# Kernel optimization log

Measured on AMD Instinct MI355X. Metric: run time of the kernel, lower is better.

Reference implementation:

```python
import jax, jax.numpy as jnp
import numpy as np

B, T, C, H = 16, 512, 256, 8
HS_T = C // H   # temporal head size = 32
HS_S = T // H   # spatial head size = 64
EPS = 1e-6


def _ln(x, w, b):
    m = x.mean(-1, keepdims=True)
    v = ((x - m) ** 2).mean(-1, keepdims=True)
    return (x - m) / jnp.sqrt(v + EPS) * w + b


def setup_inputs() -> dict:
    key = jax.random.key(0)
    ks = jax.random.split(key, 16)
    rn = lambda k, s, scale: jax.random.normal(k, s, dtype=jnp.float32) * scale
    inp = {
        "x_T": rn(ks[0], (B, T, C), 1.0),
        "x_S": rn(ks[1], (B, C, T), 1.0),
        # temporal attention: per-head q/k/v projections, stacked [H, hs, C]
        "Wq_t": rn(ks[2], (H, HS_T, C), C ** -0.5),
        "Wk_t": rn(ks[3], (H, HS_T, C), C ** -0.5),
        "Wv_t": rn(ks[4], (H, HS_T, C), C ** -0.5),
        "Wo": rn(ks[5], (C, C), C ** -0.5),
        # spatial attention: per-head q/k over the time axis, stacked [H, hs_s, T]
        "Wq_s": rn(ks[6], (H, HS_S, T), T ** -0.5),
        "Wk_s": rn(ks[7], (H, HS_S, T), T ** -0.5),
        # feed-forward blocks (expansion_factor=4)
        "ff1_w1": rn(ks[8], (4 * C, C), C ** -0.5),
        "ff1_b1": jnp.zeros((4 * C,), jnp.float32),
        "ff1_w2": rn(ks[9], (C, 4 * C), (4 * C) ** -0.5),
        "ff1_b2": jnp.zeros((C,), jnp.float32),
        "ff2_w1": rn(ks[10], (4 * C, C), C ** -0.5),
        "ff2_b1": jnp.zeros((4 * C,), jnp.float32),
        "ff2_w2": rn(ks[11], (C, 4 * C), (4 * C) ** -0.5),
        "ff2_b2": jnp.zeros((C,), jnp.float32),
        # layernorm affine params
        "t_ln1_w": jnp.ones((C,), jnp.float32), "t_ln1_b": jnp.zeros((C,), jnp.float32),
        "t_ln2_w": jnp.ones((C,), jnp.float32), "t_ln2_b": jnp.zeros((C,), jnp.float32),
        "s_ln1_w": jnp.ones((T,), jnp.float32), "s_ln1_b": jnp.zeros((T,), jnp.float32),
        "fus_ln_w": jnp.ones((C,), jnp.float32), "fus_ln_b": jnp.zeros((C,), jnp.float32),
    }
    return inp


def reference(x_T, x_S, Wq_t, Wk_t, Wv_t, Wo, Wq_s, Wk_s,
              ff1_w1, ff1_b1, ff1_w2, ff1_b2, ff2_w1, ff2_b1, ff2_w2, ff2_b2,
              t_ln1_w, t_ln1_b, t_ln2_w, t_ln2_b, s_ln1_w, s_ln1_b,
              fus_ln_w, fus_ln_b):
    # ---- temporal (causal) multi-head attention ----
    h = _ln(x_T, t_ln1_w, t_ln1_b)                         # [B,T,C]
    q = jnp.einsum('btc,hdc->bhtd', h, Wq_t)
    k = jnp.einsum('btc,hdc->bhtd', h, Wk_t)
    v = jnp.einsum('btc,hdc->bhtd', h, Wv_t)
    scores = jnp.einsum('bhtd,bhsd->bhts', q, k) / jnp.sqrt(jnp.float32(HS_T))
    causal = jnp.tril(jnp.ones((T, T), dtype=bool))
    scores = jnp.where(causal, scores, -jnp.inf)
    att = jax.nn.softmax(scores, axis=-1)
    o = jnp.einsum('bhts,bhsd->bhtd', att, v)              # [B,H,T,hs]
    o = o.transpose(0, 2, 1, 3).reshape(B, T, C)           # concat heads
    attn_out = o @ Wo.T
    x = x_T + attn_out
    # FFN 1
    h2 = _ln(x, t_ln2_w, t_ln2_b)
    f = jax.nn.relu(h2 @ ff1_w1.T + ff1_b1) @ ff1_w2.T + ff1_b2
    temporal_out = x + f                                   # [B,T,C]
    # ---- spatial (non-causal) attention over neurons ----
    hs = _ln(x_S, s_ln1_w, s_ln1_b)                        # [B,C,T]
    qs = jnp.einsum('bct,hdt->bhcd', hs, Wq_s)
    ks = jnp.einsum('bct,hdt->bhcd', hs, Wk_s)
    sc = jnp.einsum('bhcd,bhed->bhce', qs, ks) / jnp.sqrt(jnp.float32(HS_S))
    spatial_weights = jax.nn.softmax(sc, axis=-1).mean(axis=1)   # [B,C,C], mean over heads
    # ---- fusion ----
    fused = jnp.einsum('bce,bte->btc', spatial_weights, temporal_out)
    x2 = temporal_out + fused
    h3 = _ln(x2, fus_ln_w, fus_ln_b)
    f2 = jax.nn.relu(h3 @ ff2_w1.T + ff2_b1) @ ff2_w2.T + ff2_b2
    out = x2 + f2
    return out, spatial_weights
```

## Files before the change

### kernel.cpp

```cpp
#include <hip/hip_runtime.h>
#include <hip/hip_bf16.h>

typedef __hip_bfloat16 bf16;
typedef __attribute__((ext_vector_type(8))) short short8;
typedef __attribute__((ext_vector_type(4))) float f32x4;

#define F_BIAS 1
#define F_RELU 2
#define F_RES  4

__device__ __forceinline__ void st_out(float* p, float v){ *p = v; }
__device__ __forceinline__ void st_out(bf16* p, float v){ *p = __float2bfloat16(v); }
__device__ __forceinline__ short f2bs(float f){
  bf16 h = __float2bfloat16(f);
  return *reinterpret_cast<short*>(&h);
}

__device__ __forceinline__ void gl_lds16(const void* g, void* l){
  __builtin_amdgcn_global_load_lds(
      (const __attribute__((address_space(1))) void*)g,
      (__attribute__((address_space(3))) void*)l, 16, 0, 0);
}

struct ProArgs {
  const float* wsrc[10];
  bf16* wdst[10];
  const float *xT, *xS, *tl1w, *tl1b, *sl1w, *sl1b;
  bf16 *hT, *hS;
};

__device__ void ln_body(bf16* __restrict__ dst, const float* __restrict__ src,
                        const float* __restrict__ w, const float* __restrict__ bvec,
                        int row, int rowLen){
  int tid = threadIdx.x;
  const float* s = src + (size_t)row*rowLen;
  float x0 = s[tid];
  float x1 = (rowLen > 256) ? s[tid+256] : 0.0f;
  float sum = x0 + x1, sq = x0*x0 + x1*x1;
  #pragma unroll
  for (int off=32; off; off>>=1){
    sum += __shfl_down(sum, off, 64);
    sq  += __shfl_down(sq , off, 64);
  }
  __shared__ float sbs[4], sbq[4];
  int wid = tid>>6, lane = tid&63;
  if (lane==0){ sbs[wid]=sum; sbq[wid]=sq; }
  __syncthreads();
  if (tid==0){
    float a=0, b2=0;
    for (int i=0;i<4;i++){ a+=sbs[i]; b2+=sbq[i]; }
    sbs[0]=a; sbq[0]=b2;
  }
  __syncthreads();
  float inv  = 1.0f/(float)rowLen;
  float mean = sbs[0]*inv;
  float var  = sbq[0]*inv - mean*mean;
  float rstd = rsqrtf(var + 1e-6f);
  bf16* d = dst + (size_t)row*rowLen;
  d[tid] = __float2bfloat16((x0-mean)*rstd*w[tid] + bvec[tid]);
  if (rowLen > 256)
    d[tid+256] = __float2bfloat16((x1-mean)*rstd*w[tid+256] + bvec[tid+256]);
}

__global__ __launch_bounds__(256) void prologue(ProArgs a){
  int blk = blockIdx.x;
  if (blk < 1792){
    int v = blk*256 + threadIdx.x;
    int e = v*4;
    int seg = (e>=65536)+(e>=131072)+(e>=196608)+(e>=262144)+(e>=524288)
            + (e>=786432)+(e>=1048576)+(e>=1310720)+(e>=1572864);
    const int starts[10] = {0,65536,131072,196608,262144,524288,786432,
                            1048576,1310720,1572864};
    int off = e - starts[seg];
    float4 f = *(const float4*)(a.wsrc[seg] + off);
    short4 o;
    o.x = f2bs(f.x); o.y = f2bs(f.y); o.z = f2bs(f.z); o.w = f2bs(f.w);
    *(short4*)((short*)a.wdst[seg] + off) = o;
  } else if (blk < 1792 + 8192){
    ln_body(a.hT, a.xT, a.tl1w, a.tl1b, blk-1792, 256);
  } else {
    ln_body(a.hS, a.xS, a.sl1w, a.sl1b, blk-9984, 512);
  }
}

template<int BM, int BK>
__device__ __forceinline__ void gemm_body(
    const bf16* __restrict__ A, const bf16* __restrict__ B,
    float* __restrict__ outF, bf16* __restrict__ outB,
    const float* __restrict__ bias, const float* __restrict__ resid,
    int K, int lda, int ldb, int ldc, int flags, int m0, int n0){
  __shared__ short As[BM*BK];
  __shared__ short Bs[128*BK];
  int tid = threadIdx.x;
  int w = tid>>6, lane = tid&63, quad = lane>>4, l16 = lane&15;
  constexpr int WM = BM/2;
  constexpr int MF = WM/16;
  constexpr int CPR = BK/8;
  constexpr int CA = BM*CPR/256;
  constexpr int CB = 128*CPR/256;
  int wm = (w>>1)*WM, wn = (w&1)*64;
  f32x4 acc[MF][4];
  #pragma unroll
  for (int r=0;r<MF;r++)
    #pragma unroll
    for (int j=0;j<4;j++)
      acc[r][j] = (f32x4){0.f,0.f,0.f,0.f};

  for (int k0 = 0; k0 < K; k0 += BK){
    #pragma unroll
    for (int c=0;c<CA;c++){
      int ch = tid + c*256;
      int row = ch / CPR, p = ch % CPR;
      gl_lds16(A + (size_t)(m0+row)*lda + k0 + ((p ^ (row&(CPR-1)))*8),
               &As[row*BK + p*8]);
    }
    #pragma unroll
    for (int c=0;c<CB;c++){
      int ch = tid + c*256;
      int row = ch / CPR, p = ch % CPR;
      gl_lds16(B + (size_t)(n0+row)*ldb + k0 + ((p ^ (row&(CPR-1)))*8),
               &Bs[row*BK + p*8]);
    }
    __syncthreads();
    #pragma unroll
    for (int ks=0; ks<BK/32; ++ks){
      short8 af[MF], bfr[4];
      #pragma unroll
      for (int r=0;r<MF;r++){
        int rr = wm + r*16 + l16;
        af[r] = *(short8*)&As[rr*BK + (((ks*4+quad) ^ (rr&(CPR-1)))*8)];
      }
      #pragma unroll
      for (int j=0;j<4;j++){
        int rr = wn + j*16 + l16;
        bfr[j] = *(short8*)&Bs[rr*BK + (((ks*4+quad) ^ (rr&(CPR-1)))*8)];
      }
      #pragma unroll
      for (int r=0;r<MF;r++)
        #pragma unroll
        for (int j=0;j<4;j++)
          acc[r][j] = __builtin_amdgcn_mfma_f32_16x16x32_bf16(af[r], bfr[j], acc[r][j], 0,0,0);
    }
    __syncthreads();
  }
  #pragma unroll
  for (int r=0;r<MF;r++){
    int mb = m0 + wm + r*16 + quad*4;
    #pragma unroll
    for (int j=0;j<4;j++){
      int n = n0 + wn + j*16 + l16;
      float bv = (flags & F_BIAS) ? bias[n] : 0.0f;
      #pragma unroll
      for (int e=0;e<4;e++){
        float v = acc[r][j][e] + bv;
        if (flags & F_RELU) v = fmaxf(v, 0.0f);
        long long idx = (long long)(mb+e)*ldc + n;
        if (flags & F_RES) v += resid[idx];
        if (outF) outF[idx] = v;
        if (outB) st_out(outB + idx, v);
      }
    }
  }
}

template<int BM, int BK>
__global__ __launch_bounds__(256) void gemm_mfma(
    const bf16* __restrict__ A, const bf16* __restrict__ B,
    float* __restrict__ outF, bf16* __restrict__ outB,
    const float* __restrict__ bias, const float* __restrict__ resid,
    int K, int lda, int ldb, int ldc, int flags){
  gemm_body<BM,BK>(A,B,outF,outB,bias,resid,K,lda,ldb,ldc,flags,
                   blockIdx.x*BM, blockIdx.y*128);
}

struct GArgs {
  const bf16 *A, *B;
  float* outF; bf16* outB;
  const float *bias, *resid;
  int K, lda, ldb, ldc, flags, ty;
};
__global__ __launch_bounds__(256) void gemm_dual(GArgs g0, GArgs g1, int n0){
  int id = blockIdx.x;
  bool first = id < n0;
  const GArgs& g = first ? g0 : g1;
  int t = first ? id : id - n0;
  int bx = t / g.ty, by = t - bx*g.ty;
  gemm_body<128,64>(g.A, g.B, g.outF, g.outB, g.bias, g.resid,
                    g.K, g.lda, g.ldb, g.ldc, g.flags, bx*128, by*128);
}

__global__ __launch_bounds__(256) void gemm_ln(
    const bf16* __restrict__ A, const bf16* __restrict__ B,
    float* __restrict__ outF, bf16* __restrict__ outLN,
    const float* __restrict__ resid,
    const float* __restrict__ lnw, const float* __restrict__ lnb,
    int K, int lda, int ldb, int flags,
    long long sA, long long sB, long long sO, long long sR){
  int bz = blockIdx.z;
  A += (size_t)bz*sA;
  B += (size_t)bz*sB;
  long long obase = (long long)bz*sO;
  __shared__ short As[32*64];
  __shared__ short Bs[256*64];
  __shared__ float redS[2][32], redQ[2][32];
  int tid = threadIdx.x;
  int m0 = blockIdx.x*32;
  int w = tid>>6, lane = tid&63, quad = lane>>4, l16 = lane&15;
  int wm = (w>>1)*16, wn = (w&1)*128;
  f32x4 acc[8];
  #pragma unroll
  for (int j=0;j<8;j++) acc[j] = (f32x4){0.f,0.f,0.f,0.f};

  for (int k0 = 0; k0 < K; k0 += 64){
    {
      int row = tid >> 3, p = tid & 7;
      gl_lds16(A + (size_t)(m0+row)*lda + k0 + ((p ^ (row&7))*8),
               &As[row*64 + p*8]);
    }
    #pragma unroll
    for (int c=0;c<8;c++){
      int ch = tid + c*256;
      int row = ch >> 3, p = ch & 7;
      gl_lds16(B + (size_t)row*ldb + k0 + ((p ^ (row&7))*8),
               &Bs[row*64 + p*8]);
    }
    __syncthreads();
    #pragma unroll
    for (int ks=0; ks<2; ++ks){
      int rr = wm + l16;
      short8 af = *(short8*)&As[rr*64 + (((ks*4+quad) ^ (rr&7))*8)];
      #pragma unroll
      for (int j=0;j<8;j++){
        int rb = wn + j*16 + l16;
        short8 bfr = *(short8*)&Bs[rb*64 + (((ks*4+quad) ^ (rb&7))*8)];
        acc[j] = __builtin_amdgcn_mfma_f32_16x16x32_bf16(af, bfr, acc[j], 0,0,0);
      }
    }
    __syncthreads();
  }
  #pragma unroll
  for (int e=0;e<4;e++){
    int row = wm + quad*4 + e;
    float s = 0.f, q2 = 0.f;
    #pragma unroll
    for (int j=0;j<8;j++){
      float v = acc[j][e];
      if (flags & F_RES)
        v += resid[(long long)bz*sR + (long long)(m0+row)*256 + wn + j*16 + l16];
      acc[j][e] = v;
      s += v; q2 += v*v;
    }
    #pragma unroll
    for (int off=1; off<16; off<<=1){
      s  += __shfl_xor(s , off, 16);
      q2 += __shfl_xor(q2, off, 16);
    }
    if (l16==0){ redS[w&1][row] = s; redQ[w&1][row] = q2; }
  }
  __syncthreads();
  #pragma unroll
  for (int e=0;e<4;e++){
    int row = wm + quad*4 + e;
    float tot = redS[0][row] + redS[1][row];
    float tq  = redQ[0][row] + redQ[1][row];
    float mean = tot * (1.0f/256.0f);
    float var  = tq * (1.0f/256.0f) - mean*mean;
    float rstd = rsqrtf(var + 1e-6f);
    #pragma unroll
    for (int j=0;j<8;j++){
      int col = wn + j*16 + l16;
      float v = acc[j][e];
      long long idx = obase + (long long)(m0+row)*256 + col;
      if (outF) outF[idx] = v;
      outLN[idx] = __float2bfloat16((v-mean)*rstd*lnw[col] + lnb[col]);
    }
  }
}

__device__ __forceinline__ int fsw(int row){ return (row>>1)&3; }
__global__ __launch_bounds__(256) void flash_mfma(
    const bf16* __restrict__ qkv, bf16* __restrict__ o){
  int qt = (int)gridDim.x - 1 - (int)blockIdx.x;
  int h = blockIdx.y, b = blockIdx.z;
  int tid = threadIdx.x;
  int w = tid>>6, lane = tid&63, quad = lane>>4, l16 = lane&15;
  __shared__ bf16 Qs[64*32];
  __shared__ bf16 Ks[64*32];
  __shared__ bf16 Vt[32*72];
  __shared__ bf16 Ps[64*72];
  const bf16* base = qkv + (size_t)b*512*768;
  int t0 = qt*64;
  int srow = tid>>2, spos = tid&3;
  gl_lds16(base + (size_t)(t0+srow)*768 + h*32 + ((spos ^ fsw(srow))*8),
           &Qs[srow*32 + spos*8]);
  f32x4 accO[2];
  accO[0] = (f32x4){0.f,0.f,0.f,0.f};
  accO[1] = (f32x4){0.f,0.f,0.f,0.f};
  float m_i[4], l_i[4];
  #pragma unroll
  for (int e=0;e<4;e++){ m_i[e] = -3.0e38f; l_i[e] = 0.0f; }
  const float scale = 0.17677669529663687f;

  for (int kt = 0; kt <= qt; ++kt){
    int s0 = kt*64;
    __syncthreads();
    {
      const bf16* rp = base + (size_t)(s0+srow)*768 + h*32;
      gl_lds16(rp + 256 + ((spos ^ fsw(srow))*8), &Ks[srow*32 + spos*8]);
      short8 v = *(const short8*)(rp + 512 + spos*8);
      #pragma unroll
      for (int q=0;q<8;q++){
        short tmp = v[q];
        Vt[(spos*8+q)*72 + srow] = *(bf16*)&tmp;
      }
    }
    __syncthreads();
    int rq = w*16 + l16;
    short8 aq = *(short8*)&Qs[rq*32 + ((quad ^ fsw(rq))*8)];
    f32x4 S[4];
    #pragma unroll
    for (int j2=0;j2<4;j2++){
      int rk = j2*16 + l16;
      short8 bk = *(short8*)&Ks[rk*32 + ((quad ^ fsw(rk))*8)];
      S[j2] = __builtin_amdgcn_mfma_f32_16x16x32_bf16(aq, bk,
                (f32x4){0.f,0.f,0.f,0.f}, 0,0,0);
    }
    bool diag = (kt == qt);
    int qrow_base = t0 + w*16 + quad*4;
    #pragma unroll
    for (int e=0;e<4;e++){
      float sv[4];
      #pragma unroll
      for (int j2=0;j2<4;j2++){
        float x = S[j2][e]*scale;
        if (diag && (s0 + j2*16 + l16 > qrow_base + e)) x = -3.0e38f;
        sv[j2] = x;
      }
      float mx = fmaxf(fmaxf(sv[0],sv[1]), fmaxf(sv[2],sv[3]));
      #pragma unroll
      for (int off=1; off<16; off<<=1) mx = fmaxf(mx, __shfl_xor(mx, off, 64));
      float m_new = fmaxf(m_i[e], mx);
      float alpha = __expf(m_i[e]-m_new);
      float rs = 0.0f;
      #pragma unroll
      for (int j2=0;j2<4;j2++){
        float p = __expf(sv[j2]-m_new);
        rs += p;
        Ps[(w*16+quad*4+e)*72 + j2*16 + l16] = __float2bfloat16(p);
      }
      #pragma unroll
      for (int off=1; off<16; off<<=1) rs += __shfl_xor(rs, off, 64);
      l_i[e] = l_i[e]*alpha + rs;
      m_i[e] = m_new;
      accO[0][e] *= alpha;
      accO[1][e] *= alpha;
    }
    __syncthreads();
    #pragma unroll
    for (int sh=0; sh<2; ++sh){
      short8 ap = *(short8*)&Ps[(w*16+l16)*72 + sh*32 + quad*8];
      #pragma unroll
      for (int dh=0; dh<2; ++dh){
        short8 bv = *(short8*)&Vt[(dh*16+l16)*72 + sh*32 + quad*8];
        accO[dh] = __builtin_amdgcn_mfma_f32_16x16x32_bf16(ap, bv, accO[dh], 0,0,0);
      }
    }
  }
  #pragma unroll
  for (int e=0;e<4;e++){
    float inv = 1.0f/l_i[e];
    int t = t0 + w*16 + quad*4 + e;
    bf16* op = o + ((size_t)(b*512+t))*256 + h*32 + l16;
    op[0]  = __float2bfloat16(accO[0][e]*inv);
    op[16] = __float2bfloat16(accO[1][e]*inv);
  }
}

__device__ void spatial_body(const bf16* __restrict__ qk,
                             float* __restrict__ out1, bf16* __restrict__ swB,
                             int ct, int b){
  int tid = threadIdx.x;
  int w = tid>>6, lane = tid&63, quad = lane>>4, l16 = lane&15;
  __shared__ bf16 Qall[16*512];
  __shared__ bf16 Ks[256*64];
  __shared__ float redM[4][16], redS2[4][16];
  const bf16* qbase = qk + ((size_t)(b*256 + ct*16))*1024;
  #pragma unroll
  for (int c=0;c<4;c++){
    int ch = tid + c*256;
    int row = ch>>6, p = ch&63;
    gl_lds16(qbase + (size_t)row*1024 + ((p ^ (row&7))*8), &Qall[row*512 + p*8]);
  }
  float fRes[4][4];
  #pragma unroll
  for (int j=0;j<4;j++)
    #pragma unroll
    for (int e=0;e<4;e++) fRes[j][e] = 0.0f;

  for (int h=0; h<8; ++h){
    __syncthreads();
    #pragma unroll
    for (int c=0;c<8;c++){
      int ch = tid + c*256;
      int e = ch>>3, p = ch&7;
      gl_lds16(qk + ((size_t)(b*256 + e))*1024 + 512 + h*64 + ((p ^ (e&7))*8),
               &Ks[e*64 + p*8]);
    }
    __syncthreads();
    f32x4 acc[4];
    #pragma unroll
    for (int j=0;j<4;j++) acc[j] = (f32x4){0.f,0.f,0.f,0.f};
    #pragma unroll
    for (int ks=0; ks<2; ++ks){
      int g = h*8 + ks*4 + quad;
      short8 aq = *(short8*)&Qall[l16*512 + ((g ^ (l16&7))*8)];
      #pragma unroll
      for (int j=0;j<4;j++){
        int e = w*64 + j*16 + l16;
        short8 bk = *(short8*)&Ks[e*64 + (((ks*4+quad) ^ (e&7))*8)];
        acc[j] = __builtin_amdgcn_mfma_f32_16x16x32_bf16(aq, bk, acc[j], 0,0,0);
      }
    }
    #pragma unroll
    for (int e=0;e<4;e++){
      float m = -3.0e38f;
      #pragma unroll
      for (int j=0;j<4;j++){
        float s = acc[j][e]*0.125f;
        acc[j][e] = s;
        m = fmaxf(m, s);
      }
      #pragma unroll
      for (int off=1; off<16; off<<=1) m = fmaxf(m, __shfl_xor(m, off, 16));
      if (l16==0) redM[w][quad*4+e] = m;
    }
    __syncthreads();
    #pragma unroll
    for (int e=0;e<4;e++){
      int r = quad*4+e;
      float m = fmaxf(fmaxf(redM[0][r],redM[1][r]), fmaxf(redM[2][r],redM[3][r]));
      float s = 0.0f;
      #pragma unroll
      for (int j=0;j<4;j++){
        float p = __expf(acc[j][e]-m);
        acc[j][e] = p; s += p;
      }
      #pragma unroll
      for (int off=1; off<16; off<<=1) s += __shfl_xor(s, off, 16);
      if (l16==0) redS2[w][r] = s;
    }
    __syncthreads();
    #pragma unroll
    for (int e=0;e<4;e++){
      int r = quad*4+e;
      float tot = redS2[0][r]+redS2[1][r]+redS2[2][r]+redS2[3][r];
      float inv = 0.125f/tot;
      #pragma unroll
      for (int j=0;j<4;j++) fRes[j][e] += acc[j][e]*inv;
    }
  }
  #pragma unroll
  for (int e=0;e<4;e++){
    int c = ct*16 + quad*4 + e;
    size_t rb = ((size_t)b*256 + c)*256;
    #pragma unroll
    for (int j=0;j<4;j++){
      int col = w*64 + j*16 + l16;
      out1[rb+col] = fRes[j][e];
      swB[rb+col]  = __float2bfloat16(fRes[j][e]);
    }
  }
}

__global__ __launch_bounds__(256) void mixed_l2(
    const bf16* __restrict__ gA, const bf16* __restrict__ gB,
    float* __restrict__ gOutF, bf16* __restrict__ gOutB,
    const float* __restrict__ gBias, const float* __restrict__ gResid,
    const bf16* __restrict__ qk, float* __restrict__ out1,
    bf16* __restrict__ swB){
  int id = blockIdx.x;
  if (id < 256){
    int bx = id >> 1, by = id & 1;
    gemm_body<64,64>(gA, gB, gOutF, gOutB, gBias, gResid,
                     1024, 1024, 1024, 256, F_BIAS|F_RES, bx*64, by*128);
  } else {
    int t = id - 256;
    spatial_body(qk, out1, swB, t & 15, t >> 4);
  }
}

extern "C" void kernel_launch(void* const* d_in, const int* in_sizes, int n_in,
                              void* d_out, int out_size, void* d_ws, size_t ws_size,
                              hipStream_t stream){
  (void)in_sizes; (void)n_in; (void)out_size; (void)ws_size;
  const float* x_T  = (const float*)d_in[0];
  const float* x_S  = (const float*)d_in[1];
  const float* Wq_t = (const float*)d_in[2];
  const float* Wk_t = (const float*)d_in[3];
  const float* Wv_t = (const float*)d_in[4];
  const float* Wo   = (const float*)d_in[5];
  const float* Wq_s = (const float*)d_in[6];
  const float* Wk_s = (const float*)d_in[7];
  const float* f1w1 = (const float*)d_in[8];
  const float* f1b1 = (const float*)d_in[9];
  const float* f1w2 = (const float*)d_in[10];
  const float* f1b2 = (const float*)d_in[11];
  const float* f2w1 = (const float*)d_in[12];
  const float* f2b1 = (const float*)d_in[13];
  const float* f2w2 = (const float*)d_in[14];
  const float* f2b2 = (const float*)d_in[15];
  const float* tl1w = (const float*)d_in[16];
  const float* tl1b = (const float*)d_in[17];
  const float* tl2w = (const float*)d_in[18];
  const float* tl2b = (const float*)d_in[19];
  const float* sl1w = (const float*)d_in[20];
  const float* sl1b = (const float*)d_in[21];
  const float* flw  = (const float*)d_in[22];
  const float* flb  = (const float*)d_in[23];

  float* ws = (float*)d_ws;
  size_t off = 0;
  bf16*  Wqkvb  = (bf16*)(ws + off); off += 768*256/2;
  bf16*  Wob    = (bf16*)(ws + off); off += 256*256/2;
  bf16*  f1w1b  = (bf16*)(ws + off); off += 1024*256/2;
  bf16*  f1w2b  = (bf16*)(ws + off); off += 256*1024/2;
  bf16*  f2w1b  = (bf16*)(ws + off); off += 1024*256/2;
  bf16*  f2w2b  = (bf16*)(ws + off); off += 256*1024/2;
  bf16*  WSb    = (bf16*)(ws + off); off += 1024*512/2;
  bf16*  bufHb  = (bf16*)(ws + off); off += (size_t)8192*256/2;
  bf16*  bufHSb = (bf16*)(ws + off); off += (size_t)4096*512/2;
  bf16*  bufQKVb= (bf16*)(ws + off); off += (size_t)8192*768/2;
  bf16*  bufBigB= (bf16*)(ws + off); off += (size_t)8192*1024/2;
  bf16*  bufOb  = (bf16*)(ws + off); off += (size_t)8192*256/2;
  bf16*  bufTOb = (bf16*)(ws + off); off += (size_t)8192*256/2;
  bf16*  swB    = (bf16*)(ws + off); off += (size_t)16*256*256/2;
  bf16*  qkB    = (bf16*)(ws + off); off += (size_t)4096*1024/2;
  float* bufX   = ws + off; off += (size_t)8192*256;
  float* bufTO  = ws + off; off += (size_t)8192*256;
  float* bufX2  = ws + off; off += (size_t)8192*256;

  float* out0 = (float*)d_out;
  float* out1 = out0 + (size_t)16*512*256;

  ProArgs pa;
  pa.wsrc[0]=Wq_t;  pa.wdst[0]=Wqkvb;
  pa.wsrc[1]=Wk_t;  pa.wdst[1]=Wqkvb+65536;
  pa.wsrc[2]=Wv_t;  pa.wdst[2]=Wqkvb+131072;
  pa.wsrc[3]=Wo;    pa.wdst[3]=Wob;
  pa.wsrc[4]=f1w1;  pa.wdst[4]=f1w1b;
  pa.wsrc[5]=f1w2;  pa.wdst[5]=f1w2b;
  pa.wsrc[6]=f2w1;  pa.wdst[6]=f2w1b;
  pa.wsrc[7]=f2w2;  pa.wdst[7]=f2w2b;
  pa.wsrc[8]=Wq_s;  pa.wdst[8]=WSb;
  pa.wsrc[9]=Wk_s;  pa.wdst[9]=WSb+262144;
  pa.xT=x_T; pa.xS=x_S; pa.tl1w=tl1w; pa.tl1b=tl1b;
  pa.sl1w=sl1w; pa.sl1b=sl1b; pa.hT=bufHb; pa.hS=bufHSb;
  prologue<<<14080,256,0,stream>>>(pa);

  GArgs gq, gs;
  gq.A=bufHb;  gq.B=Wqkvb; gq.outF=nullptr; gq.outB=bufQKVb;
  gq.bias=nullptr; gq.resid=nullptr;
  gq.K=256; gq.lda=256; gq.ldb=256; gq.ldc=768; gq.flags=0; gq.ty=6;
  gs.A=bufHSb; gs.B=WSb;   gs.outF=nullptr; gs.outB=qkB;
  gs.bias=nullptr; gs.resid=nullptr;
  gs.K=512; gs.lda=512; gs.ldb=512; gs.ldc=1024; gs.flags=0; gs.ty=8;
  gemm_dual<<<640,256,0,stream>>>(gq, gs, 384);

  flash_mfma<<<dim3(8,8,16),256,0,stream>>>(bufQKVb, bufOb);
  gemm_ln<<<dim3(256,1,1),256,0,stream>>>(bufOb, Wob, bufX, bufHb,
        x_T, tl2w, tl2b, 256, 256,256, F_RES, 0,0,0,0);
  gemm_mfma<128,64><<<dim3(64,8),256,0,stream>>>(bufHb, f1w1b, nullptr, bufBigB,
        f1b1, nullptr, 256, 256,256,1024, F_BIAS|F_RELU);
  mixed_l2<<<512,256,0,stream>>>(bufBigB, f1w2b, bufTO, bufTOb, f1b2, bufX,
        qkB, out1, swB);
  gemm_ln<<<dim3(16,1,16),256,0,stream>>>(bufTOb, swB, bufX2, bufHb,
        bufTO, flw, flb, 256, 256,256, F_RES,
        131072, 65536, 131072, 131072);
  gemm_mfma<128,64><<<dim3(64,8),256,0,stream>>>(bufHb, f2w1b, nullptr, bufBigB,
        f2b1, nullptr, 256, 256,256,1024, F_BIAS|F_RELU);
  gemm_mfma<64,64><<<dim3(128,2),256,0,stream>>>(bufBigB, f2w2b, out0, nullptr,
        f2b2, bufX2, 1024, 1024,1024,256, F_BIAS|F_RES);
}
```

Baseline: 289.6 us.

## Double-buffer LDS in GEMM, flash and spatial kernels; wave-per-row layernorm

```diff
diff --git a/kernel.cpp b/kernel.cpp
--- a/kernel.cpp
+++ b/kernel.cpp
@@ -29,41 +29,53 @@
   bf16 *hT, *hS;
 };
 
-__device__ void ln_body(bf16* __restrict__ dst, const float* __restrict__ src,
-                        const float* __restrict__ w, const float* __restrict__ bvec,
-                        int row, int rowLen){
-  int tid = threadIdx.x;
-  const float* s = src + (size_t)row*rowLen;
-  float x0 = s[tid];
-  float x1 = (rowLen > 256) ? s[tid+256] : 0.0f;
-  float sum = x0 + x1, sq = x0*x0 + x1*x1;
+template<int RL>
+__device__ __forceinline__ void wave_ln(bf16* __restrict__ dst,
+    const float* __restrict__ src, const float* __restrict__ w,
+    const float* __restrict__ bvec, int row){
+  int lane = threadIdx.x & 63;
+  const float* s = src + (size_t)row*RL;
+  float4 v0 = *(const float4*)(s + lane*4);
+  float4 v1 = {0.f,0.f,0.f,0.f};
+  float sum = v0.x+v0.y+v0.z+v0.w;
+  float sq  = v0.x*v0.x+v0.y*v0.y+v0.z*v0.z+v0.w*v0.w;
+  if (RL == 512){
+    v1 = *(const float4*)(s + 256 + lane*4);
+    sum += v1.x+v1.y+v1.z+v1.w;
+    sq  += v1.x*v1.x+v1.y*v1.y+v1.z*v1.z+v1.w*v1.w;
+  }
   #pragma unroll
   for (int off=32; off; off>>=1){
-    sum += __shfl_down(sum, off, 64);
-    sq  += __shfl_down(sq , off, 64);
-  }
-  __shared__ float sbs[4], sbq[4];
-  int wid = tid>>6, lane = tid&63;
-  if (lane==0){ sbs[wid]=sum; sbq[wid]=sq; }
-  __syncthreads();
-  if (tid==0){
-    float a=0, b2=0;
-    for (int i=0;i<4;i++){ a+=sbs[i]; b2+=sbq[i]; }
-    sbs[0]=a; sbq[0]=b2;
-  }
-  __syncthreads();
-  float inv  = 1.0f/(float)rowLen;
-  float mean = sbs[0]*inv;
-  float var  = sbq[0]*inv - mean*mean;
-  float rstd = rsqrtf(var + 1e-6f);
-  bf16* d = dst + (size_t)row*rowLen;
-  d[tid] = __float2bfloat16((x0-mean)*rstd*w[tid] + bvec[tid]);
-  if (rowLen > 256)
-    d[tid+256] = __float2bfloat16((x1-mean)*rstd*w[tid+256] + bvec[tid+256]);
+    sum += __shfl_xor(sum, off, 64);
+    sq  += __shfl_xor(sq , off, 64);
+  }
+  const float inv = 1.0f/(float)RL;
+  float mean = sum*inv;
+  float rstd = rsqrtf(sq*inv - mean*mean + 1e-6f);
+  float4 w0 = *(const float4*)(w + lane*4);
+  float4 b0 = *(const float4*)(bvec + lane*4);
+  bf16* d = dst + (size_t)row*RL;
+  short4 o;
+  o.x = f2bs((v0.x-mean)*rstd*w0.x + b0.x);
+  o.y = f2bs((v0.y-mean)*rstd*w0.y + b0.y);
+  o.z = f2bs((v0.z-mean)*rstd*w0.z + b0.z);
+  o.w = f2bs((v0.w-mean)*rstd*w0.w + b0.w);
+  *(short4*)((short*)d + lane*4) = o;
+  if (RL == 512){
+    float4 w1 = *(const float4*)(w + 256 + lane*4);
+    float4 b1 = *(const float4*)(bvec + 256 + lane*4);
+    short4 o1;
+    o1.x = f2bs((v1.x-mean)*rstd*w1.x + b1.x);
+    o1.y = f2bs((v1.y-mean)*rstd*w1.y + b1.y);
+    o1.z = f2bs((v1.z-mean)*rstd*w1.z + b1.z);
+    o1.w = f2bs((v1.w-mean)*rstd*w1.w + b1.w);
+    *(short4*)((short*)d + 256 + lane*4) = o1;
+  }
 }
 
 __global__ __launch_bounds__(256) void prologue(ProArgs a){
   int blk = blockIdx.x;
+  int wid = threadIdx.x >> 6;
   if (blk < 1792){
     int v = blk*256 + threadIdx.x;
     int e = v*4;
@@ -76,21 +88,20 @@
     short4 o;
     o.x = f2bs(f.x); o.y = f2bs(f.y); o.z = f2bs(f.z); o.w = f2bs(f.w);
     *(short4*)((short*)a.wdst[seg] + off) = o;
-  } else if (blk < 1792 + 8192){
-    ln_body(a.hT, a.xT, a.tl1w, a.tl1b, blk-1792, 256);
+  } else if (blk < 1792 + 2048){
+    wave_ln<256>(a.hT, a.xT, a.tl1w, a.tl1b, (blk-1792)*4 + wid);
   } else {
-    ln_body(a.hS, a.xS, a.sl1w, a.sl1b, blk-9984, 512);
+    wave_ln<512>(a.hS, a.xS, a.sl1w, a.sl1b, (blk-3840)*4 + wid);
   }
 }
 
 template<int BM, int BK>
 __device__ __forceinline__ void gemm_body(
+    short* __restrict__ AsB, short* __restrict__ BsB,
     const bf16* __restrict__ A, const bf16* __restrict__ B,
     float* __restrict__ outF, bf16* __restrict__ outB,
     const float* __restrict__ bias, const float* __restrict__ resid,
     int K, int lda, int ldb, int ldc, int flags, int m0, int n0){
-  __shared__ short As[BM*BK];
-  __shared__ short Bs[128*BK];
   int tid = threadIdx.x;
   int w = tid>>6, lane = tid&63, quad = lane>>4, l16 = lane&15;
   constexpr int WM = BM/2;
@@ -106,34 +117,44 @@
     for (int j=0;j<4;j++)
       acc[r][j] = (f32x4){0.f,0.f,0.f,0.f};
 
-  for (int k0 = 0; k0 < K; k0 += BK){
+  auto stage = [&](int k0, int half){
+    short* as = AsB + half*(BM*BK);
+    short* bs = BsB + half*(128*BK);
     #pragma unroll
     for (int c=0;c<CA;c++){
       int ch = tid + c*256;
       int row = ch / CPR, p = ch % CPR;
       gl_lds16(A + (size_t)(m0+row)*lda + k0 + ((p ^ (row&(CPR-1)))*8),
-               &As[row*BK + p*8]);
+               &as[row*BK + p*8]);
     }
     #pragma unroll
     for (int c=0;c<CB;c++){
       int ch = tid + c*256;
       int row = ch / CPR, p = ch % CPR;
       gl_lds16(B + (size_t)(n0+row)*ldb + k0 + ((p ^ (row&(CPR-1)))*8),
-               &Bs[row*BK + p*8]);
-    }
-    __syncthreads();
+               &bs[row*BK + p*8]);
+    }
+  };
+
+  stage(0, 0);
+  __syncthreads();
+  int nk = K / BK;
+  for (int t = 0; t < nk; ++t){
+    if (t+1 < nk) stage((t+1)*BK, (t+1)&1);
+    const short* as = AsB + (t&1)*(BM*BK);
+    const short* bs = BsB + (t&1)*(128*BK);
     #pragma unroll
     for (int ks=0; ks<BK/32; ++ks){
       short8 af[MF], bfr[4];
       #pragma unroll
       for (int r=0;r<MF;r++){
         int rr = wm + r*16 + l16;
-        af[r] = *(short8*)&As[rr*BK + (((ks*4+quad) ^ (rr&(CPR-1)))*8)];
+        af[r] = *(short8*)&as[rr*BK + (((ks*4+quad) ^ (rr&(CPR-1)))*8)];
       }
       #pragma unroll
       for (int j=0;j<4;j++){
         int rr = wn + j*16 + l16;
-        bfr[j] = *(short8*)&Bs[rr*BK + (((ks*4+quad) ^ (rr&(CPR-1)))*8)];
+        bfr[j] = *(short8*)&bs[rr*BK + (((ks*4+quad) ^ (rr&(CPR-1)))*8)];
       }
       #pragma unroll
       for (int r=0;r<MF;r++)
@@ -169,7 +190,9 @@
     float* __restrict__ outF, bf16* __restrict__ outB,
     const float* __restrict__ bias, const float* __restrict__ resid,
     int K, int lda, int ldb, int ldc, int flags){
-  gemm_body<BM,BK>(A,B,outF,outB,bias,resid,K,lda,ldb,ldc,flags,
+  __shared__ __align__(16) short As[2*BM*BK];
+  __shared__ __align__(16) short Bs[2*128*BK];
+  gemm_body<BM,BK>(As,Bs,A,B,outF,outB,bias,resid,K,lda,ldb,ldc,flags,
                    blockIdx.x*BM, blockIdx.y*128);
 }
 
@@ -180,12 +203,14 @@
   int K, lda, ldb, ldc, flags, ty;
 };
 __global__ __launch_bounds__(256) void gemm_dual(GArgs g0, GArgs g1, int n0){
+  __shared__ __align__(16) short As[2*128*64];
+  __shared__ __align__(16) short Bs[2*128*64];
   int id = blockIdx.x;
   bool first = id < n0;
   const GArgs& g = first ? g0 : g1;
   int t = first ? id : id - n0;
   int bx = t / g.ty, by = t - bx*g.ty;
-  gemm_body<128,64>(g.A, g.B, g.outF, g.outB, g.bias, g.resid,
+  gemm_body<128,64>(As, Bs, g.A, g.B, g.outF, g.outB, g.bias, g.resid,
                     g.K, g.lda, g.ldb, g.ldc, g.flags, bx*128, by*128);
 }
 
@@ -200,8 +225,8 @@
   A += (size_t)bz*sA;
   B += (size_t)bz*sB;
   long long obase = (long long)bz*sO;
-  __shared__ short As[32*64];
-  __shared__ short Bs[256*64];
+  __shared__ __align__(16) short As[2*32*64];
+  __shared__ __align__(16) short Bs[2*256*64];
   __shared__ float redS[2][32], redQ[2][32];
   int tid = threadIdx.x;
   int m0 = blockIdx.x*32;
@@ -211,28 +236,38 @@
   #pragma unroll
   for (int j=0;j<8;j++) acc[j] = (f32x4){0.f,0.f,0.f,0.f};
 
-  for (int k0 = 0; k0 < K; k0 += 64){
+  auto stage = [&](int k0, int half){
+    short* as = As + half*(32*64);
+    short* bs = Bs + half*(256*64);
     {
       int row = tid >> 3, p = tid & 7;
       gl_lds16(A + (size_t)(m0+row)*lda + k0 + ((p ^ (row&7))*8),
-               &As[row*64 + p*8]);
+               &as[row*64 + p*8]);
     }
     #pragma unroll
     for (int c=0;c<8;c++){
       int ch = tid + c*256;
       int row = ch >> 3, p = ch & 7;
       gl_lds16(B + (size_t)row*ldb + k0 + ((p ^ (row&7))*8),
-               &Bs[row*64 + p*8]);
-    }
-    __syncthreads();
+               &bs[row*64 + p*8]);
+    }
+  };
+
+  stage(0, 0);
+  __syncthreads();
+  int nk = K / 64;
+  for (int t = 0; t < nk; ++t){
+    if (t+1 < nk) stage((t+1)*64, (t+1)&1);
+    const short* as = As + (t&1)*(32*64);
+    const short* bs = Bs + (t&1)*(256*64);
     #pragma unroll
     for (int ks=0; ks<2; ++ks){
       int rr = wm + l16;
-      short8 af = *(short8*)&As[rr*64 + (((ks*4+quad) ^ (rr&7))*8)];
+      short8 af = *(short8*)&as[rr*64 + (((ks*4+quad) ^ (rr&7))*8)];
       #pragma unroll
       for (int j=0;j<8;j++){
         int rb = wn + j*16 + l16;
-        short8 bfr = *(short8*)&Bs[rb*64 + (((ks*4+quad) ^ (rb&7))*8)];
+        short8 bfr = *(short8*)&bs[rb*64 + (((ks*4+quad) ^ (rb&7))*8)];
         acc[j] = __builtin_amdgcn_mfma_f32_16x16x32_bf16(af, bfr, acc[j], 0,0,0);
       }
     }
@@ -284,15 +319,25 @@
   int h = blockIdx.y, b = blockIdx.z;
   int tid = threadIdx.x;
   int w = tid>>6, lane = tid&63, quad = lane>>4, l16 = lane&15;
-  __shared__ bf16 Qs[64*32];
-  __shared__ bf16 Ks[64*32];
-  __shared__ bf16 Vt[32*72];
-  __shared__ bf16 Ps[64*72];
+  __shared__ __align__(16) bf16 Qs[64*32];
+  __shared__ __align__(16) bf16 Ks[2][64*32];
+  __shared__ __align__(16) bf16 Vt[2][32*72];
+  __shared__ __align__(16) bf16 Ps[64*72];
   const bf16* base = qkv + (size_t)b*512*768;
   int t0 = qt*64;
   int srow = tid>>2, spos = tid&3;
   gl_lds16(base + (size_t)(t0+srow)*768 + h*32 + ((spos ^ fsw(srow))*8),
            &Qs[srow*32 + spos*8]);
+  {
+    const bf16* rp = base + (size_t)srow*768 + h*32;
+    gl_lds16(rp + 256 + ((spos ^ fsw(srow))*8), &Ks[0][srow*32 + spos*8]);
+    short8 v = *(const short8*)(rp + 512 + spos*8);
+    #pragma unroll
+    for (int q=0;q<8;q++){
+      short tmp = v[q];
+      Vt[0][(spos*8+q)*72 + srow] = *(bf16*)&tmp;
+    }
+  }
   f32x4 accO[2];
   accO[0] = (f32x4){0.f,0.f,0.f,0.f};
   accO[1] = (f32x4){0.f,0.f,0.f,0.f};
@@ -300,32 +345,29 @@
   #pragma unroll
   for (int e=0;e<4;e++){ m_i[e] = -3.0e38f; l_i[e] = 0.0f; }
   const float scale = 0.17677669529663687f;
+  __syncthreads();
+  int rq = w*16 + l16;
+  short8 aq = *(short8*)&Qs[rq*32 + ((quad ^ fsw(rq))*8)];
 
   for (int kt = 0; kt <= qt; ++kt){
-    int s0 = kt*64;
-    __syncthreads();
-    {
-      const bf16* rp = base + (size_t)(s0+srow)*768 + h*32;
-      gl_lds16(rp + 256 + ((spos ^ fsw(srow))*8), &Ks[srow*32 + spos*8]);
-      short8 v = *(const short8*)(rp + 512 + spos*8);
-      #pragma unroll
-      for (int q=0;q<8;q++){
-        short tmp = v[q];
-        Vt[(spos*8+q)*72 + srow] = *(bf16*)&tmp;
-      }
-    }
-    __syncthreads();
-    int rq = w*16 + l16;
-    short8 aq = *(short8*)&Qs[rq*32 + ((quad ^ fsw(rq))*8)];
+    int cur = kt&1, nxt = cur^1;
+    bool pre = (kt < qt);
+    short8 vpre;
+    if (pre){
+      const bf16* rp = base + (size_t)((kt+1)*64 + srow)*768 + h*32;
+      gl_lds16(rp + 256 + ((spos ^ fsw(srow))*8), &Ks[nxt][srow*32 + spos*8]);
+      vpre = *(const short8*)(rp + 512 + spos*8);
+    }
     f32x4 S[4];
     #pragma unroll
     for (int j2=0;j2<4;j2++){
       int rk = j2*16 + l16;
-      short8 bk = *(short8*)&Ks[rk*32 + ((quad ^ fsw(rk))*8)];
+      short8 bk = *(short8*)&Ks[cur][rk*32 + ((quad ^ fsw(rk))*8)];
       S[j2] = __builtin_amdgcn_mfma_f32_16x16x32_bf16(aq, bk,
                 (f32x4){0.f,0.f,0.f,0.f}, 0,0,0);
     }
     bool diag = (kt == qt);
+    int s0 = kt*64;
     int qrow_base = t0 + w*16 + quad*4;
     #pragma unroll
     for (int e=0;e<4;e++){
@@ -355,16 +397,25 @@
       accO[0][e] *= alpha;
       accO[1][e] *= alpha;
     }
-    __syncthreads();
+    asm volatile("s_waitcnt lgkmcnt(0)" ::: "memory");
+    __builtin_amdgcn_sched_barrier(0);
     #pragma unroll
     for (int sh=0; sh<2; ++sh){
       short8 ap = *(short8*)&Ps[(w*16+l16)*72 + sh*32 + quad*8];
       #pragma unroll
       for (int dh=0; dh<2; ++dh){
-        short8 bv = *(short8*)&Vt[(dh*16+l16)*72 + sh*32 + quad*8];
+        short8 bv = *(short8*)&Vt[cur][(dh*16+l16)*72 + sh*32 + quad*8];
         accO[dh] = __builtin_amdgcn_mfma_f32_16x16x32_bf16(ap, bv, accO[dh], 0,0,0);
       }
     }
+    if (pre){
+      #pragma unroll
+      for (int q=0;q<8;q++){
+        short tmp = vpre[q];
+        Vt[nxt][(spos*8+q)*72 + srow] = *(bf16*)&tmp;
+      }
+    }
+    __syncthreads();
   }
   #pragma unroll
   for (int e=0;e<4;e++){
@@ -376,13 +427,12 @@
   }
 }
 
-__device__ void spatial_body(const bf16* __restrict__ qk,
+__device__ void spatial_body(bf16* __restrict__ Qall, bf16* __restrict__ KsB,
+                             const bf16* __restrict__ qk,
                              float* __restrict__ out1, bf16* __restrict__ swB,
                              int ct, int b){
   int tid = threadIdx.x;
   int w = tid>>6, lane = tid&63, quad = lane>>4, l16 = lane&15;
-  __shared__ bf16 Qall[16*512];
-  __shared__ bf16 Ks[256*64];
   __shared__ float redM[4][16], redS2[4][16];
   const bf16* qbase = qk + ((size_t)(b*256 + ct*16))*1024;
   #pragma unroll
@@ -391,33 +441,38 @@
     int row = ch>>6, p = ch&63;
     gl_lds16(qbase + (size_t)row*1024 + ((p ^ (row&7))*8), &Qall[row*512 + p*8]);
   }
-  float fRes[4][4];
-  #pragma unroll
-  for (int j=0;j<4;j++)
-    #pragma unroll
-    for (int e=0;e<4;e++) fRes[j][e] = 0.0f;
-
-  for (int h=0; h<8; ++h){
-    __syncthreads();
+  auto stageK = [&](int h, int half){
+    bf16* ks = KsB + half*(256*64);
     #pragma unroll
     for (int c=0;c<8;c++){
       int ch = tid + c*256;
       int e = ch>>3, p = ch&7;
       gl_lds16(qk + ((size_t)(b*256 + e))*1024 + 512 + h*64 + ((p ^ (e&7))*8),
-               &Ks[e*64 + p*8]);
-    }
-    __syncthreads();
+               &ks[e*64 + p*8]);
+    }
+  };
+  stageK(0, 0);
+  float fRes[4][4];
+  #pragma unroll
+  for (int j=0;j<4;j++)
+    #pragma unroll
+    for (int e=0;e<4;e++) fRes[j][e] = 0.0f;
+  __syncthreads();
+
+  for (int h=0; h<8; ++h){
+    if (h < 7) stageK(h+1, (h+1)&1);
+    const bf16* kcur = KsB + (h&1)*(256*64);
     f32x4 acc[4];
     #pragma unroll
     for (int j=0;j<4;j++) acc[j] = (f32x4){0.f,0.f,0.f,0.f};
     #pragma unroll
-    for (int ks=0; ks<2; ++ks){
-      int g = h*8 + ks*4 + quad;
+    for (int ki=0; ki<2; ++ki){
+      int g = h*8 + ki*4 + quad;
       short8 aq = *(short8*)&Qall[l16*512 + ((g ^ (l16&7))*8)];
       #pragma unroll
       for (int j=0;j<4;j++){
         int e = w*64 + j*16 + l16;
-        short8 bk = *(short8*)&Ks[e*64 + (((ks*4+quad) ^ (e&7))*8)];
+        short8 bk = *(short8*)&kcur[e*64 + (((ki*4+quad) ^ (e&7))*8)];
         acc[j] = __builtin_amdgcn_mfma_f32_16x16x32_bf16(aq, bk, acc[j], 0,0,0);
       }
     }
@@ -478,14 +533,15 @@
     const float* __restrict__ gBias, const float* __restrict__ gResid,
     const bf16* __restrict__ qk, float* __restrict__ out1,
     bf16* __restrict__ swB){
+  __shared__ __align__(16) short lds[40960];
   int id = blockIdx.x;
   if (id < 256){
     int bx = id >> 1, by = id & 1;
-    gemm_body<64,64>(gA, gB, gOutF, gOutB, gBias, gResid,
+    gemm_body<64,64>(lds, lds + 2*64*64, gA, gB, gOutF, gOutB, gBias, gResid,
                      1024, 1024, 1024, 256, F_BIAS|F_RES, bx*64, by*128);
   } else {
     int t = id - 256;
-    spatial_body(qk, out1, swB, t & 15, t >> 4);
+    spatial_body((bf16*)lds, (bf16*)(lds + 8192), qk, out1, swB, t & 15, t >> 4);
   }
 }
 
@@ -555,7 +611,7 @@
   pa.wsrc[9]=Wk_s;  pa.wdst[9]=WSb+262144;
   pa.xT=x_T; pa.xS=x_S; pa.tl1w=tl1w; pa.tl1b=tl1b;
   pa.sl1w=sl1w; pa.sl1b=sl1b; pa.hT=bufHb; pa.hS=bufHSb;
-  prologue<<<14080,256,0,stream>>>(pa);
+  prologue<<<4864,256,0,stream>>>(pa);
 
   GArgs gq, gs;
   gq.A=bufHb;  gq.B=Wqkvb; gq.outF=nullptr; gq.outB=bufQKVb;
```

New measurement: 303.4 us. 4.8% more time.
